# Kernel optimization log

Hardware: AMD Instinct MI355X
Metric: run time of the kernel (lower is better)

## Reference

```python
import jax, jax.numpy as jnp
import numpy as np

NUM_EMBEDDINGS = 8192
EMBEDDING_DIM = 256
COMMITMENT_COST = 0.25


def setup_inputs() -> dict:
    key = jax.random.key(0)
    k1, k2 = jax.random.split(key)
    hidden_states = jax.random.normal(k1, (16, EMBEDDING_DIM, 32, 32), dtype=jnp.float32)
    # nn.Embedding init: uniform(-1/K, 1/K)
    emb_weights = jax.random.uniform(
        k2, (NUM_EMBEDDINGS, EMBEDDING_DIM), dtype=jnp.float32,
        minval=-1.0 / NUM_EMBEDDINGS, maxval=1.0 / NUM_EMBEDDINGS)
    return {"hidden_states": hidden_states, "emb_weights": emb_weights}


def reference(hidden_states, emb_weights):
    # (B, C, H, W) -> (B, H, W, C) -> (N, C)
    h = jnp.transpose(hidden_states, (0, 2, 3, 1))
    flat = h.reshape(-1, EMBEDDING_DIM)
    # squared L2 distance to every codebook entry: (N, K)
    distance = (jnp.sum(flat * flat, axis=1, keepdims=True)
                + jnp.sum(emb_weights * emb_weights, axis=1)
                - 2.0 * flat @ emb_weights.T)
    min_encoding_indices = jnp.argmin(distance, axis=1)  # (N,)
    # direct gather (same math as one-hot @ codebook in the original)
    z_q = emb_weights[min_encoding_indices].reshape(h.shape)  # (B, H, W, C)
    # return_loss=True path
    loss = (jnp.mean((jax.lax.stop_gradient(z_q) - h) ** 2)
            + COMMITMENT_COST * jnp.mean((z_q - jax.lax.stop_gradient(h)) ** 2))
    # straight-through estimator
    z_q = h + jax.lax.stop_gradient(z_q - h)
    z_q = jnp.transpose(z_q, (0, 3, 1, 2))  # back to (B, C, H, W)
    min_encoding_indices = min_encoding_indices.reshape(h.shape[0], -1)
    return z_q, min_encoding_indices, loss
```

## Files before the change

kernel.cpp:

```cpp
#include <hip/hip_runtime.h>


#define N_ROWS 16384
#define K_CAND 8192
#define CDIM   256
#define NELEM  4194304

#define SA_FLT   0
#define SK_FLT   16384
#define SL_FLT   49152
#define SQC_FLT  49160
#define SBB_FLT  51208
#define SQ_FLT   59400
#define SFB_FLT  1337352
#define SEB_FLT  3434504
#define QCAP     624

typedef __attribute__((ext_vector_type(8))) short short8;
typedef __attribute__((ext_vector_type(4))) float f32x4;
typedef __attribute__((ext_vector_type(4))) unsigned uint32x4;

__device__ __forceinline__ unsigned short f2bf_rne(float x) {
    unsigned u = __float_as_uint(x);
    return (unsigned short)((u + 0x7fffu + ((u >> 16) & 1u)) >> 16);
}
__device__ __forceinline__ float bf2f(unsigned short u) {
    return __uint_as_float(((unsigned)u) << 16);
}
__device__ __forceinline__ unsigned ordU(float f) {
    unsigned u = __float_as_uint(f);
    return u ^ (((int)u >> 31) | 0x80000000u);
}

__global__ void kA(const float* __restrict__ hs, float* __restrict__ out) {
    float* A = out + SA_FLT;
    unsigned long long* keys = (unsigned long long*)(out + SK_FLT);
    int n = blockIdx.x * 64 + threadIdx.x;
    keys[n] = ~0ull;
    if (n == 0) *(double*)(out + SL_FLT) = 0.0;
    int b = n >> 10, yx = n & 1023;
    const float* base = hs + ((size_t)b << 18) + yx;
    float hsum[2];
    for (int h = 0; h < 2; ++h) {
        float r[8];
        #pragma unroll
        for (int j = 0; j < 8; ++j) {
            float x = base[(size_t)(h * 128 + j) << 10];
            r[j] = __fmul_rn(x, x);
        }
        for (int i = 8; i < 128; i += 8) {
            #pragma unroll
            for (int j = 0; j < 8; ++j) {
                float x = base[(size_t)(h * 128 + i + j) << 10];
                r[j] = __fadd_rn(r[j], __fmul_rn(x, x));
            }
        }
        hsum[h] = __fadd_rn(
            __fadd_rn(__fadd_rn(r[0], r[1]), __fadd_rn(r[2], r[3])),
            __fadd_rn(__fadd_rn(r[4], r[5]), __fadd_rn(r[6], r[7])));
    }
    A[n] = __fadd_rn(hsum[0], hsum[1]);
}

__global__ void kFbf(const float* __restrict__ hs, float* __restrict__ out) {
    unsigned short* fbf = (unsigned short*)(out + SFB_FLT);
    __shared__ float T[64][65];
    int blk = blockIdx.x;
    int b = blk >> 6, cB = (blk >> 4) & 3, yB = blk & 15;
    int t = threadIdx.x;
    int yl = t & 63, ch = t >> 6;
    const float* src = hs + ((size_t)b << 18) + (((size_t)cB * 64) << 10) + yB * 64 + yl;
    #pragma unroll
    for (int i = 0; i < 16; ++i) {
        int c = ch * 16 + i;
        T[c][yl] = src[(size_t)c << 10];
    }
    __syncthreads();
    int yr = t >> 2, cs = (t & 3) * 16;
    short8 v0, v1;
    #pragma unroll
    for (int j = 0; j < 8; ++j) {
        v0[j] = (short)f2bf_rne(2.0f * T[cs + j][yr]);
        v1[j] = (short)f2bf_rne(2.0f * T[cs + 8 + j][yr]);
    }
    unsigned short* dst = fbf + (((size_t)(b * 1024 + yB * 64 + yr)) << 8) + cB * 64 + cs;
    *(short8*)dst = v0;
    *(short8*)(dst + 8) = v1;
}

__global__ void kEbf(const float* __restrict__ emb, float* __restrict__ out) {
    unsigned short* ebf = (unsigned short*)(out + SEB_FLT);
    float* bbfNeg = out + SBB_FLT;
    int cand = blockIdx.x * 64 + threadIdx.x;
    const float* ep = emb + ((size_t)cand << 8);
    unsigned short* dp = ebf + (((size_t)(cand >> 4)) << 12) + (cand & 15) * 8;
    float s = 0.f;
    for (int c0 = 0; c0 < 256; c0 += 8) {
        short8 v;
        #pragma unroll
        for (int j = 0; j < 8; ++j) {
            unsigned short bb = f2bf_rne(ep[c0 + j]);
            v[j] = (short)bb;
            float eh = bf2f(bb);
            s = fmaf(eh, eh, s);
        }
        *(short8*)(dp + (c0 >> 3) * 128) = v;
    }
    bbfNeg[cand] = -s;
}

__global__ __launch_bounds__(256, 3) void kScr(const float* __restrict__ hs,
                                               const float* __restrict__ emb,
                                               float* __restrict__ out) {
    const float* A = out + SA_FLT;
    unsigned* qcount = (unsigned*)(out + SQC_FLT);
    const float* bbfNeg = out + SBB_FLT;
    unsigned* queue = (unsigned*)(out + SQ_FLT);
    const unsigned short* fbf = (const unsigned short*)(out + SFB_FLT);
    const unsigned short* ebf = (const unsigned short*)(out + SEB_FLT);

    __shared__ __align__(16) short As[64][264];
    __shared__ unsigned rowMaxOrd[64];
    __shared__ float margLds[64];
    __shared__ int lqnH[2];

    const int t = threadIdx.x, blk = blockIdx.x;
    const int row0 = (blk >> 2) * 64;
    const int candSplit = (blk & 3) * 2048;
    const int lane = t & 63, wid = t >> 6;
    const int quad = lane >> 4, l15 = lane & 15;
    const int qb0 = (blk >> 2) * 8 + (blk & 3);
    unsigned* qB[2] = { queue + (size_t)qb0 * QCAP,
                        queue + (size_t)(qb0 + 4) * QCAP };

    if (t < 64) {
        rowMaxOrd[t] = 0u;
        margLds[t] = 2.0e-5f * sqrtf(A[row0 + t]) + 4.0e-5f;
    }
    if (t < 2) lqnH[t] = 0;

    {
        const unsigned short* src = fbf + ((size_t)row0 << 8);
        #pragma unroll
        for (int i = 0; i < 8; ++i) {
            int idx = (i * 256 + t) * 8;
            short8 v = *(const short8*)(src + idx);
            *(short8*)&As[idx >> 8][idx & 255] = v;
        }
    }
    __syncthreads();

    f32x4 mgv[4];
    #pragma unroll
    for (int m = 0; m < 4; ++m)
        mgv[m] = *(const f32x4*)&margLds[m * 16 + quad * 4];

    for (int cc = 0; cc < 8; ++cc) {
        const int candW = candSplit + cc * 256 + wid * 64;
        const unsigned short* ebW = ebf + (((size_t)candW) << 8)
                                       + quad * 128 + l15 * 8;
        f32x4 acc[4][4];
        #pragma unroll
        for (int jc = 0; jc < 4; ++jc) {
            float bneg = bbfNeg[candW + jc * 16 + l15];
            #pragma unroll
            for (int m = 0; m < 4; ++m)
                acc[m][jc] = (f32x4){bneg, bneg, bneg, bneg};
        }
        #pragma unroll
        for (int ks = 0; ks < 8; ++ks) {
            short8 bf[4];
            #pragma unroll
            for (int jc = 0; jc < 4; ++jc)
                bf[jc] = *(const short8*)(ebW + jc * 4096 + ks * 512);
            #pragma unroll
            for (int m = 0; m < 4; ++m) {
                short8 af = *(const short8*)&As[m * 16 + l15][ks * 32 + quad * 8];
                #pragma unroll
                for (int jc = 0; jc < 4; ++jc)
                    acc[m][jc] = __builtin_amdgcn_mfma_f32_16x16x32_bf16(
                        af, bf[jc], acc[m][jc], 0, 0, 0);
            }
        }
        #pragma unroll
        for (int m = 0; m < 4; ++m) {
            uint32x4 thv = *(const uint32x4*)&rowMaxOrd[m * 16 + quad * 4];
            #pragma unroll
            for (int reg = 0; reg < 4; ++reg) {
                int rl = m * 16 + quad * 4 + reg;
                float vmax = fmaxf(fmaxf(acc[m][0][reg], acc[m][1][reg]),
                                   fmaxf(acc[m][2][reg], acc[m][3][reg]));
                unsigned th = thv[reg];
                float mg = mgv[m][reg];
                bool hot = ordU(__fadd_rn(vmax, mg)) >= th;
                unsigned long long bal = __ballot(hot);
                if (((bal >> (quad * 16)) & 0xFFFFull) == 0ull) continue;
                float g = vmax;
                g = fmaxf(g, __shfl_xor(g, 1, 16));
                g = fmaxf(g, __shfl_xor(g, 2, 16));
                g = fmaxf(g, __shfl_xor(g, 4, 16));
                g = fmaxf(g, __shfl_xor(g, 8, 16));
                unsigned og = ordU(g);
                if (og > th) { atomicMax(&rowMaxOrd[rl], og); th = og; }
                #pragma unroll
                for (int jc = 0; jc < 4; ++jc) {
                    float x = acc[m][jc][reg];
                    if (ordU(__fadd_rn(x, mg)) >= th) {
                        int slot = atomicAdd(&lqnH[m >> 1], 1);
                        if (slot < QCAP)
                            qB[m >> 1][slot] = ((unsigned)(rl & 31) << 13)
                                             | (unsigned)(candW + jc * 16 + l15);
                    }
                }
            }
        }
    }
    __syncthreads();
    if (t < 2) qcount[qb0 + t * 4] = (unsigned)lqnH[t];
}

__global__ __launch_bounds__(256, 4) void kTailE(const float* __restrict__ hs,
                                                 const float* __restrict__ emb,
                                                 float* __restrict__ out) {
    const float* A = out + SA_FLT;
    unsigned long long* keys = (unsigned long long*)(out + SK_FLT);
    const unsigned* qcount = (const unsigned*)(out + SQC_FLT);
    const unsigned* queue = (const unsigned*)(out + SQ_FLT);

    __shared__ __align__(16) float F[32][260];

    const int t = threadIdx.x, blk = blockIdx.x;
    const int row0 = (blk >> 2) * 32;
    const unsigned* qBlk = queue + (size_t)blk * QCAP;

    int n = (int)qcount[blk];
    if (n == 0) return;

    {
        int yl = t & 31, cq = t >> 5;
        int nrow = row0 + yl;
        int b = nrow >> 10, yx = nrow & 1023;
        const float* src = hs + ((size_t)b << 18) + yx;
        #pragma unroll
        for (int i = 0; i < 32; ++i) {
            int c = i * 8 + cq;
            F[yl][c] = src[(size_t)c << 10];
        }
    }
    __syncthreads();

    if (n > QCAP) {
        int cb = (blk & 3) * 2048;
        for (int p = t; p < 32 * 2048; p += 256) {
            int rl = p >> 11, cand = cb + (p & 2047);
            const float* ep = emb + ((size_t)cand << 8);
            float acc = 0.f;
            #pragma unroll 8
            for (int c0 = 0; c0 < 256; c0 += 4) {
                f32x4 f4 = *(const f32x4*)&F[rl][c0];
                f32x4 e4 = *(const f32x4*)(ep + c0);
                acc = fmaf(f4[0], e4[0], acc);
                acc = fmaf(f4[1], e4[1], acc);
                acc = fmaf(f4[2], e4[2], acc);
                acc = fmaf(f4[3], e4[3], acc);
            }
            int row = row0 + rl;
            float d = __fsub_rn(A[row], __fadd_rn(acc, acc));
            unsigned long long key =
                ((unsigned long long)__float_as_uint(d) << 32) | (unsigned)cand;
            atomicMin(&keys[row], key);
        }
        return;
    }

    for (int i = t; i < n; i += 256) {
        unsigned e = qBlk[i];
        int rl = (int)(e >> 13), cand = (int)(e & 8191u);
        const float* ep = emb + ((size_t)cand << 8);
        float acc = 0.f;
        #pragma unroll 8
        for (int c0 = 0; c0 < 256; c0 += 4) {
            f32x4 f4 = *(const f32x4*)&F[rl][c0];
            f32x4 e4 = *(const f32x4*)(ep + c0);
            acc = fmaf(f4[0], e4[0], acc);
            acc = fmaf(f4[1], e4[1], acc);
            acc = fmaf(f4[2], e4[2], acc);
            acc = fmaf(f4[3], e4[3], acc);
        }
        int row = row0 + rl;
        float d = __fsub_rn(A[row], __fadd_rn(acc, acc));
        unsigned long long key =
            ((unsigned long long)__float_as_uint(d) << 32) | (unsigned)cand;
        atomicMin(&keys[row], key);
    }
}

__global__ void kPost(float* __restrict__ out) {
    const unsigned long long* keys = (const unsigned long long*)(out + SK_FLT);
    double* lossAcc = (double*)(out + SL_FLT);
    __shared__ double sd[256];
    int n = blockIdx.x * 256 + threadIdx.x;
    unsigned long long key = keys[n];
    unsigned idx = (unsigned)(key & 0xffffffffu) & 8191u;
    float d = __uint_as_float((unsigned)(key >> 32));
    out[NELEM + n] = (float)idx;
    sd[threadIdx.x] = (double)d;
    __syncthreads();
    for (int s = 128; s > 0; s >>= 1) {
        if (threadIdx.x < s) sd[threadIdx.x] += sd[threadIdx.x + s];
        __syncthreads();
    }
    if (threadIdx.x == 0) atomicAdd(lossAcc, sd[0]);
}

__global__ void kLoss(float* __restrict__ out) {
    if (threadIdx.x == 0) {
        double loss = 1.25 * (*(const double*)(out + SL_FLT)) / (double)NELEM;
        out[NELEM + N_ROWS] = (float)loss;
    }
}

__global__ void kZQ(const float* __restrict__ hs, const float* __restrict__ emb,
                    float* __restrict__ out) {
    int o = blockIdx.x * 256 + threadIdx.x;
    int n = (o & 1023) | ((o >> 18) << 10);
    int c = (o >> 10) & 255;
    unsigned idx = (unsigned)out[NELEM + n] & 8191u;
    float e = emb[((size_t)idx << 8) + c];
    float h = hs[o];
    out[o] = __fadd_rn(h, __fsub_rn(e, h));
}

extern "C" void kernel_launch(void* const* d_in, const int* in_sizes, int n_in,
                              void* d_out, int out_size, void* d_ws, size_t ws_size,
                              hipStream_t stream) {
    const float* hs  = (const float*)d_in[0];
    const float* emb = (const float*)d_in[1];
    float* out = (float*)d_out;

    kA<<<N_ROWS / 64, 64, 0, stream>>>(hs, out);
    kFbf<<<1024, 256, 0, stream>>>(hs, out);
    kEbf<<<K_CAND / 64, 64, 0, stream>>>(emb, out);
    kScr<<<1024, 256, 0, stream>>>(hs, emb, out);
    kTailE<<<2048, 256, 0, stream>>>(hs, emb, out);
    kPost<<<N_ROWS / 256, 256, 0, stream>>>(out);
    kLoss<<<1, 64, 0, stream>>>(out);
    kZQ<<<NELEM / 256, 256, 0, stream>>>(hs, emb, out);
}
```

Baseline: 355.4 us.

## Tile codebook gather in kZQ via LDS, widen kA/kEbf blocks, move bias add

Rewrites the z_q kernel so each block gathers 64 selected codebook rows with vectorized loads into a padded LDS tile, then writes the channel-major output coalesced. Before, each thread did a scalar gather of emb with strided addresses. Also changes kA and kEbf to 256-thread blocks, and in kScr adds the negative bias after the MFMA instead of seeding the accumulators. That last change alters rounding order slightly and could shift candidate selection near ties.

New measurement: 349.9 us. Within noise of the previous version (-1.6%).

```diff
diff --git a/kernel.cpp b/kernel.cpp
--- a/kernel.cpp
+++ b/kernel.cpp
@@ -35,7 +35,7 @@
 __global__ void kA(const float* __restrict__ hs, float* __restrict__ out) {
     float* A = out + SA_FLT;
     unsigned long long* keys = (unsigned long long*)(out + SK_FLT);
-    int n = blockIdx.x * 64 + threadIdx.x;
+    int n = blockIdx.x * 256 + threadIdx.x;
     keys[n] = ~0ull;
     if (n == 0) *(double*)(out + SL_FLT) = 0.0;
     int b = n >> 10, yx = n & 1023;
@@ -91,7 +91,7 @@
 __global__ void kEbf(const float* __restrict__ emb, float* __restrict__ out) {
     unsigned short* ebf = (unsigned short*)(out + SEB_FLT);
     float* bbfNeg = out + SBB_FLT;
-    int cand = blockIdx.x * 64 + threadIdx.x;
+    int cand = blockIdx.x * 256 + threadIdx.x;
     const float* ep = emb + ((size_t)cand << 8);
     unsigned short* dp = ebf + (((size_t)(cand >> 4)) << 12) + (cand & 15) * 8;
     float s = 0.f;
@@ -159,14 +159,17 @@
         const int candW = candSplit + cc * 256 + wid * 64;
         const unsigned short* ebW = ebf + (((size_t)candW) << 8)
                                        + quad * 128 + l15 * 8;
+        float bneg[4];
+        #pragma unroll
+        for (int jc = 0; jc < 4; ++jc)
+            bneg[jc] = bbfNeg[candW + jc * 16 + l15];
+
         f32x4 acc[4][4];
         #pragma unroll
-        for (int jc = 0; jc < 4; ++jc) {
-            float bneg = bbfNeg[candW + jc * 16 + l15];
+        for (int jc = 0; jc < 4; ++jc)
             #pragma unroll
             for (int m = 0; m < 4; ++m)
-                acc[m][jc] = (f32x4){bneg, bneg, bneg, bneg};
-        }
+                acc[m][jc] = (f32x4){0.f, 0.f, 0.f, 0.f};
         #pragma unroll
         for (int ks = 0; ks < 8; ++ks) {
             short8 bf[4];
@@ -188,8 +191,11 @@
             #pragma unroll
             for (int reg = 0; reg < 4; ++reg) {
                 int rl = m * 16 + quad * 4 + reg;
-                float vmax = fmaxf(fmaxf(acc[m][0][reg], acc[m][1][reg]),
-                                   fmaxf(acc[m][2][reg], acc[m][3][reg]));
+                float x0 = __fadd_rn(acc[m][0][reg], bneg[0]);
+                float x1 = __fadd_rn(acc[m][1][reg], bneg[1]);
+                float x2 = __fadd_rn(acc[m][2][reg], bneg[2]);
+                float x3 = __fadd_rn(acc[m][3][reg], bneg[3]);
+                float vmax = fmaxf(fmaxf(x0, x1), fmaxf(x2, x3));
                 unsigned th = thv[reg];
                 float mg = mgv[m][reg];
                 bool hot = ordU(__fadd_rn(vmax, mg)) >= th;
@@ -202,10 +208,10 @@
                 g = fmaxf(g, __shfl_xor(g, 8, 16));
                 unsigned og = ordU(g);
                 if (og > th) { atomicMax(&rowMaxOrd[rl], og); th = og; }
+                float xs[4] = {x0, x1, x2, x3};
                 #pragma unroll
                 for (int jc = 0; jc < 4; ++jc) {
-                    float x = acc[m][jc][reg];
-                    if (ordU(__fadd_rn(x, mg)) >= th) {
+                    if (ordU(__fadd_rn(xs[jc], mg)) >= th) {
                         int slot = atomicAdd(&lqnH[m >> 1], 1);
                         if (slot < QCAP)
                             qB[m >> 1][slot] = ((unsigned)(rl & 31) << 13)
@@ -320,15 +326,45 @@
     }
 }
 
-__global__ void kZQ(const float* __restrict__ hs, const float* __restrict__ emb,
-                    float* __restrict__ out) {
-    int o = blockIdx.x * 256 + threadIdx.x;
-    int n = (o & 1023) | ((o >> 18) << 10);
-    int c = (o >> 10) & 255;
-    unsigned idx = (unsigned)out[NELEM + n] & 8191u;
-    float e = emb[((size_t)idx << 8) + c];
-    float h = hs[o];
-    out[o] = __fadd_rn(h, __fsub_rn(e, h));
+__global__ __launch_bounds__(256) void kZQ(const float* __restrict__ hs,
+                                           const float* __restrict__ emb,
+                                           float* __restrict__ out) {
+    __shared__ float E[64][65];
+    __shared__ unsigned idxL[64];
+
+    const int t = threadIdx.x, blk = blockIdx.x;
+    const int nt = blk >> 2, ct = blk & 3;
+    const int row0 = nt * 64, c0 = ct * 64;
+    const int b = row0 >> 10, yx0 = row0 & 1023;
+
+    if (t < 64) idxL[t] = (unsigned)out[NELEM + row0 + t] & 8191u;
+    __syncthreads();
+
+    {
+        int r = t >> 2, j = t & 3;
+        const float* ep = emb + ((size_t)idxL[r] << 8) + c0 + j * 16;
+        #pragma unroll
+        for (int q = 0; q < 4; ++q) {
+            f32x4 v = *(const f32x4*)(ep + q * 4);
+            #pragma unroll
+            for (int i = 0; i < 4; ++i)
+                E[j * 16 + q * 4 + i][r] = v[i];
+        }
+    }
+    __syncthreads();
+
+    {
+        int yl = t & 63, ch = t >> 6;
+        #pragma unroll
+        for (int i = 0; i < 16; ++i) {
+            int cl = ch * 16 + i;
+            size_t o = ((size_t)b << 18) | ((size_t)(c0 + cl) << 10)
+                     | (size_t)(yx0 + yl);
+            float h = hs[o];
+            float e = E[cl][yl];
+            out[o] = __fadd_rn(h, __fsub_rn(e, h));
+        }
+    }
 }
 
 extern "C" void kernel_launch(void* const* d_in, const int* in_sizes, int n_in,
@@ -338,12 +374,12 @@
     const float* emb = (const float*)d_in[1];
     float* out = (float*)d_out;
 
-    kA<<<N_ROWS / 64, 64, 0, stream>>>(hs, out);
+    kA<<<N_ROWS / 256, 256, 0, stream>>>(hs, out);
     kFbf<<<1024, 256, 0, stream>>>(hs, out);
-    kEbf<<<K_CAND / 64, 64, 0, stream>>>(emb, out);
+    kEbf<<<K_CAND / 256, 256, 0, stream>>>(emb, out);
     kScr<<<1024, 256, 0, stream>>>(hs, emb, out);
     kTailE<<<2048, 256, 0, stream>>>(hs, emb, out);
     kPost<<<N_ROWS / 256, 256, 0, stream>>>(out);
     kLoss<<<1, 64, 0, stream>>>(out);
-    kZQ<<<NELEM / 256, 256, 0, stream>>>(hs, emb, out);
-}
+    kZQ<<<1024, 256, 0, stream>>>(hs, emb, out);
+}
```
